# Optimization experiments

Measured on AMD Instinct MI355X. Metric: run time of the kernel, lower is better.

The kernel has to match this reference:

```python
import jax, jax.numpy as jnp
import numpy as np

# dims: F=N_fault, V=N_train (noise samples), E=batch, M=n_in+2, N=n_out
F, V, E, N_IN, N_OUT = 2, 4, 2048, 512, 512
M = N_IN + 2
GMIN, GMAX, EPS_TRAIN, PGMIN = 0.01, 10.0, 0.1, 1e-4
ETA2_ACT1 = 0.20  # ACT1.eta_fault[0,2], used in theta init
# pTanh activation params per ACT: a = e0 + e1*tanh((z-e2)*e3)
ETAS = np.array([[0.05, 0.90, 0.20, 8.0],
                 [0.10, 0.80, 0.30, 5.0],
                 [0.00, 1.00, 0.25, 10.0],
                 [0.15, 0.70, 0.15, 6.0]], dtype=np.float32)


def setup_inputs() -> dict:
    key = jax.random.key(0)
    k1, k2, k3, k4, k5 = jax.random.split(key, 5)
    a_previous = jax.random.uniform(k1, (F, V, E, N_IN), jnp.float32)
    # theta init per __init__: rand/100 + gmin; last row += gmax; row -2 from eta_2 formula
    theta = jax.random.uniform(k2, (M, N_OUT), jnp.float32) / 100.0 + GMIN
    theta = theta.at[-1, :].add(GMAX)
    theta = theta.at[-2, :].set(ETA2_ACT1 / (1.0 - ETA2_ACT1) * (jnp.sum(theta[:-2, :], 0) + theta[-1, :]))
    cofficients_act = jax.random.uniform(k3, (4, N_OUT), jnp.float32)
    noise_u = jax.random.uniform(k4, (F, V, M, N_OUT), jnp.float32)   # theta_noisy uniform draw
    gumbel_u = jax.random.uniform(k5, (4, N_OUT), jnp.float32)        # gumbel uniform draw
    return {"a_previous": a_previous, "theta_": theta,
            "cofficients_act": cofficients_act, "noise_u": noise_u, "gumbel_u": gumbel_u}


def _forward(a_previous, theta_, cofficients_act, noise_u, gumbel_u):
    sg = jax.lax.stop_gradient
    # --- theta property: clamp to [-gmax,gmax], zero |.|<gmin, straight-through ---
    th_c = jnp.clip(theta_, -GMAX, GMAX)
    th_t = jnp.where(jnp.abs(th_c) < GMIN, 0.0, th_c)
    theta = sg(th_t) + theta_ - sg(theta_)
    # --- theta_noisy: multiplicative uniform noise in [1-eps, 1+eps]; FaultMask == 1 ---
    theta_noisy = theta[None, None] * ((noise_u * 2.0 - 1.0) * EPS_TRAIN + 1.0)  # [F,V,M,N]
    absn = jnp.abs(theta_noisy)
    W = absn / (jnp.sum(absn, axis=2, keepdims=True) + 1e-10)
    pos = (theta_noisy >= 0).astype(theta_noisy.dtype)
    neg = 1.0 - pos
    # --- MAC: extend input with [ones, zeros], inverter path, split-sign matmul ---
    ones = jnp.ones(a_previous.shape[:3] + (1,), a_previous.dtype)
    zeros = jnp.zeros_like(ones)
    x_ext = jnp.concatenate([a_previous, ones, zeros], axis=3)  # [F,V,E,M]
    x_neg = (-x_ext).at[..., -1].set(0.0)                       # ideal INV(a) = -a, last col zeroed
    z = (jnp.einsum('fvem,fvmn->fven', x_ext, W * pos)
         + jnp.einsum('fvem,fvmn->fven', x_neg, W * neg))       # [F,V,E,N]
    # --- MAC_power: vectorized form of the quad loop ---
    # Power = sum_{f,v,m,n} g[m,n] * sum_e (x_ext*pos + x_neg*neg - y)^2 / (E*V*F)
    # pos*neg = 0, pos^2 = pos  =>  expand the square into einsum reductions.
    g_init = jnp.abs(th_c)
    g_tilde = g_init * (PGMIN / jnp.min(g_init, axis=0, keepdims=True))
    pos_d, neg_d = sg(pos), sg(neg)  # detached in torch source
    sx2 = jnp.einsum('fvem,fvem->fvm', x_ext, x_ext)
    sn2 = jnp.einsum('fvem,fvem->fvm', x_neg, x_neg)
    sy2 = jnp.einsum('fven,fven->fvn', z, z)
    C = jnp.einsum('fvem,fven->fvmn', x_ext, z)
    D = jnp.einsum('fvem,fven->fvmn', x_neg, z)
    p1 = (jnp.einsum('fvm,fvmn,mn->', sx2, pos_d, g_tilde)
          + jnp.einsum('fvm,fvmn,mn->', sn2, neg_d, g_tilde))
    p2 = -2.0 * (jnp.einsum('fvmn,fvmn,mn->', C, pos_d, g_tilde)
                 + jnp.einsum('fvmn,fvmn,mn->', D, neg_d, g_tilde))
    p3 = jnp.einsum('fvn,n->', sy2, jnp.sum(g_tilde, axis=0))
    mac_power = (p1 + p2 + p3) / (E * V * F)
    # --- CoFF_ACT: clamped logits + gumbel, softmax, hard argmax straight-through ---
    c = cofficients_act + sg(jnp.clip(cofficients_act, -1.0, 1.0) - cofficients_act)
    gn = -jnp.log(-jnp.log(gumbel_u + 1e-20) + 1e-20)
    alpha = jax.nn.softmax((c + gn) / 1.0, axis=0)              # temperature = 1.0
    hard = jax.nn.one_hot(jnp.argmax(alpha, axis=0), 4, axis=0, dtype=alpha.dtype)
    alpha_st = sg(hard) + alpha - sg(alpha)                      # [4, N]
    # --- mix the four pTanh activations ---
    a_new = jnp.zeros_like(z)
    for i in range(4):
        e0, e1, e2, e3 = ETAS[i]
        a_new = a_new + alpha_st[i] * (e0 + e1 * jnp.tanh((z - e2) * e3))
    return a_new, mac_power


def reference(a_previous, theta_, cofficients_act, noise_u, gumbel_u):
    return _forward(a_previous, theta_, cofficients_act, noise_u, gumbel_u)
```

## Files before the change

kernel.cpp:

```cpp
#include <hip/hip_runtime.h>

typedef unsigned short u16;
typedef __attribute__((ext_vector_type(8))) short short8;
typedef __attribute__((ext_vector_type(4))) float f32x4;

#define NF 2
#define NV 4
#define FV 8
#define NE 2048
#define NIN 512
#define NOUT 512
#define NM 514

#define WS_P1      0u
#define WS_P2      2048u
#define WS_P3      3072u
#define WS_SCALE   4096u
#define WS_G       6144u
#define WS_GN      8320u
#define WS_ETA     10368u
#define WS_DENOM   18560u
#define WS_BIASZ   34944u
#define WS_BIAST   51328u
#define WS_PMIN    67712u
#define WS_PSUM    198784u
#define WS_ABF     329856u
#define WS_BZT     17107072u
#define WS_BTT     21301376u

__constant__ float c_etas[4][4] = {
    {0.05f, 0.90f, 0.20f, 8.0f},
    {0.10f, 0.80f, 0.30f, 5.0f},
    {0.00f, 1.00f, 0.25f, 10.0f},
    {0.15f, 0.70f, 0.15f, 6.0f}};

__device__ __forceinline__ u16 f2bf(float x) {
    unsigned u = __float_as_uint(x);
    unsigned r = (u + 0x7fffu + ((u >> 16) & 1u)) >> 16;
    return (u16)r;
}

__device__ __forceinline__ void gll16(const void* g, void* l) {
    __builtin_amdgcn_global_load_lds((__attribute__((address_space(1))) void*)g,
                                     (__attribute__((address_space(3))) void*)l,
                                     16, 0, 0);
}

__global__ void kA_part(const float* __restrict__ theta_, float* __restrict__ pmin,
                        float* __restrict__ psum) {
    int t = threadIdx.x;
    int n2 = t * 2;
    int r0 = blockIdx.x * 9;
    float mn0 = 3.4e38f, mn1 = 3.4e38f, s0 = 0.f, s1 = 0.f;
    int rend = r0 + 9;
    if (rend > NM) rend = NM;
    for (int r = r0; r < rend; r++) {
        float2 v = *(const float2*)(theta_ + r * NOUT + n2);
        float a0 = fabsf(fminf(fmaxf(v.x, -10.f), 10.f));
        float a1 = fabsf(fminf(fmaxf(v.y, -10.f), 10.f));
        mn0 = fminf(mn0, a0); mn1 = fminf(mn1, a1);
        s0 += a0; s1 += a1;
    }
    *(float2*)(pmin + blockIdx.x * NOUT + n2) = make_float2(mn0, mn1);
    *(float2*)(psum + blockIdx.x * NOUT + n2) = make_float2(s0, s1);
}

__global__ void kB_fold(const float* __restrict__ pmin, const float* __restrict__ psum,
                        float* __restrict__ scale, float* __restrict__ Gn) {
    int n = threadIdx.x;
    float mn = 3.4e38f, s = 0.f;
    for (int i = 0; i < 64; i++) {
        mn = fminf(mn, pmin[i * NOUT + n]);
        s += psum[i * NOUT + n];
    }
    float sc = 1e-4f / mn;
    scale[n] = sc;
    Gn[n] = sc * s;
}

__global__ void kC_grow(const float* __restrict__ theta_, const float* __restrict__ scale,
                        float* __restrict__ G) {
    int m = blockIdx.x;
    int t = threadIdx.x;
    const float4* rowp = (const float4*)(theta_ + m * NOUT);
    const float4* scp = (const float4*)scale;
    float acc = 0.f;
#pragma unroll
    for (int i = 0; i < 2; i++) {
        float4 v = rowp[t * 2 + i];
        float4 s = scp[t * 2 + i];
        acc += fabsf(fminf(fmaxf(v.x, -10.f), 10.f)) * s.x
             + fabsf(fminf(fmaxf(v.y, -10.f), 10.f)) * s.y
             + fabsf(fminf(fmaxf(v.z, -10.f), 10.f)) * s.z
             + fabsf(fminf(fmaxf(v.w, -10.f), 10.f)) * s.w;
    }
    for (int off = 32; off > 0; off >>= 1) acc += __shfl_down(acc, off);
    if (t == 0) G[m] = acc;
}

__global__ void k_etasel(const float* __restrict__ coeff, const float* __restrict__ gumb,
                         float4* __restrict__ eta4) {
    int n = blockIdx.x * 256 + threadIdx.x;
    if (n >= NOUT) return;
    float best = -1e30f;
    int bi = 0;
    for (int i = 0; i < 4; i++) {
        float c = fminf(fmaxf(coeff[i * NOUT + n], -1.f), 1.f);
        float u = gumb[i * NOUT + n];
        float g = -logf(-logf(u + 1e-20f) + 1e-20f);
        float v = c + g;
        if (v > best) { best = v; bi = i; }
    }
    eta4[n] = make_float4(c_etas[bi][0], c_etas[bi][1], c_etas[bi][2], c_etas[bi][3]);
}

__global__ void k_denom(const float* __restrict__ theta_, const float* __restrict__ noise,
                        float* __restrict__ denom) {
    int fv = blockIdx.z, mc = blockIdx.y, nc = blockIdx.x;
    int t = threadIdx.x;
    int nl = t & 63, mg = t >> 6;
    int n = nc * 64 + nl;
    int mbase = mc * 128 + mg * 32;
    float acc = 0.f;
    for (int i = 0; i < 32; i++) {
        int m = mbase + i;
        if (m < NM) {
            float fac = noise[(fv * NM + m) * NOUT + n] * 0.2f + 0.9f;
            float thc = fminf(fmaxf(theta_[m * NOUT + n], -10.f), 10.f);
            float tht = (fabsf(thc) < 0.01f) ? 0.f : thc;
            acc += fabsf(tht * fac);
        }
    }
    __shared__ float red[256];
    red[t] = acc;
    __syncthreads();
    if (t < 64)
        atomicAdd(&denom[fv * NOUT + n], red[t] + red[t + 64] + red[t + 128] + red[t + 192]);
}

__global__ void k_wmat(const float* __restrict__ theta_, const float* __restrict__ scale,
                       const float* __restrict__ noise, const float* __restrict__ denom,
                       u16* __restrict__ BzT, u16* __restrict__ BtT,
                       float* __restrict__ bias_z, float* __restrict__ bias_t) {
    int fv = blockIdx.z, mt = blockIdx.y, nt = blockIdx.x;
    int t = threadIdx.x;
    int nl = t & 63, rg = t >> 6;
    __shared__ u16 Wl[64][68];
    __shared__ u16 Sl[64][68];
    int n = nt * 64 + nl;
    float rdv = 1.f / (denom[fv * NOUT + n] + 1e-10f);
    float sc = scale[n];
    for (int r = 0; r < 16; r++) {
        int ml = rg * 16 + r;
        int m = mt * 64 + ml;
        if (m < 513) {
            float fac = noise[(fv * NM + m) * NOUT + n] * 0.2f + 0.9f;
            float thc = fminf(fmaxf(theta_[m * NOUT + n], -10.f), 10.f);
            float gi = fabsf(thc);
            float tht = (gi < 0.01f) ? 0.f : thc;
            float th = tht * fac;
            float sg = (th >= 0.f) ? 1.f : -1.f;
            float gt = gi * sc;
            if (m == 512) {
                bias_z[fv * NOUT + n] = th * rdv;
                bias_t[fv * NOUT + n] = sg * gt;
            } else {
                Wl[ml][nl] = f2bf(th * rdv);
                Sl[ml][nl] = f2bf(sg * gt);
            }
        }
    }
    __syncthreads();
    if (mt < 8) {
        for (int r = 0; r < 16; r++) {
            int nl2 = rg * 16 + r;
            int ml2 = t & 63;
            int gidx = (fv * NOUT + nt * 64 + nl2) * NIN + mt * 64 + ml2;
            BzT[gidx] = Wl[ml2][nl2];
            BtT[gidx] = Sl[ml2][nl2];
        }
    }
}

__global__ void k_prepA(const float* __restrict__ a_prev, const float* __restrict__ G,
                        u16* __restrict__ Abf, float* __restrict__ p1slot) {
    int t = threadIdx.x;
    float acc = 0.f;
#pragma unroll
    for (int i = 0; i < 4; i++) {
        int idx = (i * 2048 + blockIdx.x) * 256 + t;
        float4 v = ((const float4*)a_prev)[idx];
        int k = (idx & 127) << 2;
        float4 g4 = *((const float4*)(G + k));
        acc += v.x * v.x * g4.x + v.y * v.y * g4.y + v.z * v.z * g4.z + v.w * v.w * g4.w;
        ushort4 o;
        o.x = f2bf(v.x); o.y = f2bf(v.y); o.z = f2bf(v.z); o.w = f2bf(v.w);
        ((ushort4*)Abf)[idx] = o;
    }
    for (int off = 32; off > 0; off >>= 1) acc += __shfl_down(acc, off);
    __shared__ float red[4];
    int lane = t & 63, wv = t >> 6;
    if (lane == 0) red[wv] = acc;
    __syncthreads();
    if (t == 0)
        atomicAdd(&p1slot[(blockIdx.x & 63) * 8], red[0] + red[1] + red[2] + red[3]);
}

__global__ __launch_bounds__(256, 2) void k_gemm(
    const u16* __restrict__ Abf, const u16* __restrict__ BzT, const u16* __restrict__ BtT,
    const float* __restrict__ bias_z, const float* __restrict__ bias_t,
    const float* __restrict__ Gn, const float4* __restrict__ eta4,
    float* __restrict__ out, float* __restrict__ p2slot, float* __restrict__ p3slot) {
    __shared__ alignas(16) u16 As[128 * 32];
    __shared__ alignas(16) u16 Bzs[128 * 32];
    __shared__ alignas(16) u16 Bts[128 * 32];
    const int tid = threadIdx.x;
    const int lane = tid & 63;
    const int wv = tid >> 6;
    const int wr = wv >> 1, wc = wv & 1;
    const int fv = blockIdx.z;
    const int e0 = blockIdx.y * 128;
    const int n0 = blockIdx.x * 128;

    const u16* Ag = Abf + (fv * NE + e0) * NIN;
    const u16* Bzg = BzT + (fv * NOUT + n0) * NIN;
    const u16* Btg = BtT + (fv * NOUT + n0) * NIN;

    f32x4 accz[4][4], acct[4][4];
#pragma unroll
    for (int i = 0; i < 4; i++)
#pragma unroll
        for (int j = 0; j < 4; j++) {
            f32x4 zz = {0.f, 0.f, 0.f, 0.f};
            accz[i][j] = zz;
            acct[i][j] = zz;
        }

    const int r0 = tid >> 2;
    const int c0 = (tid & 3) * 8;

    for (int k0 = 0; k0 < 512; k0 += 32) {
        gll16(Ag + r0 * 512 + k0 + c0, (u16*)As + tid * 8);
        gll16(Ag + (r0 + 64) * 512 + k0 + c0, (u16*)As + tid * 8 + 2048);
        gll16(Bzg + r0 * 512 + k0 + c0, (u16*)Bzs + tid * 8);
        gll16(Bzg + (r0 + 64) * 512 + k0 + c0, (u16*)Bzs + tid * 8 + 2048);
        gll16(Btg + r0 * 512 + k0 + c0, (u16*)Bts + tid * 8);
        gll16(Btg + (r0 + 64) * 512 + k0 + c0, (u16*)Bts + tid * 8 + 2048);
        __builtin_amdgcn_s_waitcnt(0);
        __syncthreads();
        const int kof = (lane >> 4) * 8;
        const int rA = wr * 64 + (lane & 15);
        const int rB = wc * 64 + (lane & 15);
        short8 af[4], bzf[4], btf[4];
#pragma unroll
        for (int i = 0; i < 4; i++) af[i] = *(const short8*)(As + (rA + i * 16) * 32 + kof);
#pragma unroll
        for (int j = 0; j < 4; j++) {
            bzf[j] = *(const short8*)(Bzs + (rB + j * 16) * 32 + kof);
            btf[j] = *(const short8*)(Bts + (rB + j * 16) * 32 + kof);
        }
#pragma unroll
        for (int i = 0; i < 4; i++)
#pragma unroll
            for (int j = 0; j < 4; j++) {
                accz[i][j] = __builtin_amdgcn_mfma_f32_16x16x32_bf16(af[i], bzf[j], accz[i][j], 0, 0, 0);
                acct[i][j] = __builtin_amdgcn_mfma_f32_16x16x32_bf16(af[i], btf[j], acct[i][j], 0, 0, 0);
            }
        __syncthreads();
    }

    float p2 = 0.f, p3 = 0.f;
    const int col = lane & 15;
    const int rowq = (lane >> 4) * 4;
#pragma unroll
    for (int j = 0; j < 4; j++) {
        int n = n0 + wc * 64 + j * 16 + col;
        float bz = bias_z[fv * NOUT + n];
        float bt = bias_t[fv * NOUT + n];
        float gnv = Gn[n];
        float4 e4 = eta4[n];
#pragma unroll
        for (int i = 0; i < 4; i++) {
            int ebase = e0 + wr * 64 + i * 16 + rowq;
#pragma unroll
            for (int r = 0; r < 4; r++) {
                float z = accz[i][j][r] + bz;
                float t = acct[i][j][r] + bt;
                p2 += z * t;
                p3 += z * z * gnv;
                float x = (z - e4.z) * e4.w;
                float ex = __expf(2.f * x);
                float th = 1.f - 2.f / (ex + 1.f);
                out[(fv * NE + ebase + r) * NOUT + n] = e4.x + e4.y * th;
            }
        }
    }
    for (int off = 32; off > 0; off >>= 1) {
        p2 += __shfl_down(p2, off);
        p3 += __shfl_down(p3, off);
    }
    __shared__ float r2[4], r3[4];
    if (lane == 0) { r2[wv] = p2; r3[wv] = p3; }
    __syncthreads();
    if (tid == 0) {
        int slot = ((blockIdx.x + blockIdx.y * 4 + blockIdx.z * 64) & 31) * 8;
        atomicAdd(&p2slot[slot], r2[0] + r2[1] + r2[2] + r2[3]);
        atomicAdd(&p3slot[slot], r3[0] + r3[1] + r3[2] + r3[3]);
    }
}

__global__ void k_final(const float* __restrict__ p1s, const float* __restrict__ p2s,
                        const float* __restrict__ p3s, const float* __restrict__ G,
                        float* __restrict__ out) {
    int t = threadIdx.x;
    float s1 = p1s[t * 8];
    float s2 = (t < 32) ? p2s[t * 8] : 0.f;
    float s3 = (t < 32) ? p3s[t * 8] : 0.f;
    for (int off = 32; off > 0; off >>= 1) {
        s1 += __shfl_down(s1, off);
        s2 += __shfl_down(s2, off);
        s3 += __shfl_down(s3, off);
    }
    if (t == 0) {
        float mp = (s1 + 16384.f * G[512] - 2.f * s2 + s3) * (1.f / 16384.f);
        out[8388608] = mp;
    }
}

extern "C" void kernel_launch(void* const* d_in, const int* in_sizes, int n_in,
                              void* d_out, int out_size, void* d_ws, size_t ws_size,
                              hipStream_t stream) {
    const float* a_prev = (const float*)d_in[0];
    const float* theta_ = (const float*)d_in[1];
    const float* coeff = (const float*)d_in[2];
    const float* noise = (const float*)d_in[3];
    const float* gumb = (const float*)d_in[4];
    float* out = (float*)d_out;
    char* w = (char*)d_ws;
    float* p1s = (float*)(w + WS_P1);
    float* p2s = (float*)(w + WS_P2);
    float* p3s = (float*)(w + WS_P3);
    float* scale = (float*)(w + WS_SCALE);
    float* G = (float*)(w + WS_G);
    float* Gn = (float*)(w + WS_GN);
    float4* eta4 = (float4*)(w + WS_ETA);
    float* denom = (float*)(w + WS_DENOM);
    float* bias_z = (float*)(w + WS_BIASZ);
    float* bias_t = (float*)(w + WS_BIAST);
    float* pmin = (float*)(w + WS_PMIN);
    float* psum = (float*)(w + WS_PSUM);
    u16* Abf = (u16*)(w + WS_ABF);
    u16* BzT = (u16*)(w + WS_BZT);
    u16* BtT = (u16*)(w + WS_BTT);

    hipMemsetAsync(w + WS_P1, 0, 4096, stream);
    hipMemsetAsync(w + WS_DENOM, 0, 16384, stream);

    kA_part<<<64, 256, 0, stream>>>(theta_, pmin, psum);
    kB_fold<<<1, 512, 0, stream>>>(pmin, psum, scale, Gn);
    kC_grow<<<514, 64, 0, stream>>>(theta_, scale, G);
    k_etasel<<<2, 256, 0, stream>>>(coeff, gumb, eta4);
    k_denom<<<dim3(8, 5, FV), 256, 0, stream>>>(theta_, noise, denom);
    k_wmat<<<dim3(8, 9, FV), 256, 0, stream>>>(theta_, scale, noise, denom,
                                               BzT, BtT, bias_z, bias_t);
    k_prepA<<<2048, 256, 0, stream>>>(a_prev, G, Abf, p1s);
    k_gemm<<<dim3(4, 16, FV), 256, 0, stream>>>(Abf, BzT, BtT, bias_z, bias_t, Gn, eta4,
                                                out, p2s, p3s);
    k_final<<<1, 64, 0, stream>>>(p1s, p2s, p3s, G, out);
}
```

Measured before the change: 165.1 us.

## Fuse denominator and weight-matrix kernels, merge eta selection, raise GEMM occupancy

```diff
diff --git a/kernel.cpp b/kernel.cpp
--- a/kernel.cpp
+++ b/kernel.cpp
@@ -19,9 +19,8 @@
 #define WS_G       6144u
 #define WS_GN      8320u
 #define WS_ETA     10368u
-#define WS_DENOM   18560u
-#define WS_BIASZ   34944u
-#define WS_BIAST   51328u
+#define WS_BIASZ   18560u
+#define WS_BIAST   34944u
 #define WS_PMIN    67712u
 #define WS_PSUM    198784u
 #define WS_ABF     329856u
@@ -66,7 +65,9 @@
 }
 
 __global__ void kB_fold(const float* __restrict__ pmin, const float* __restrict__ psum,
-                        float* __restrict__ scale, float* __restrict__ Gn) {
+                        const float* __restrict__ coeff, const float* __restrict__ gumb,
+                        float* __restrict__ scale, float* __restrict__ Gn,
+                        float4* __restrict__ eta4) {
     int n = threadIdx.x;
     float mn = 3.4e38f, s = 0.f;
     for (int i = 0; i < 64; i++) {
@@ -76,32 +77,6 @@
     float sc = 1e-4f / mn;
     scale[n] = sc;
     Gn[n] = sc * s;
-}
-
-__global__ void kC_grow(const float* __restrict__ theta_, const float* __restrict__ scale,
-                        float* __restrict__ G) {
-    int m = blockIdx.x;
-    int t = threadIdx.x;
-    const float4* rowp = (const float4*)(theta_ + m * NOUT);
-    const float4* scp = (const float4*)scale;
-    float acc = 0.f;
-#pragma unroll
-    for (int i = 0; i < 2; i++) {
-        float4 v = rowp[t * 2 + i];
-        float4 s = scp[t * 2 + i];
-        acc += fabsf(fminf(fmaxf(v.x, -10.f), 10.f)) * s.x
-             + fabsf(fminf(fmaxf(v.y, -10.f), 10.f)) * s.y
-             + fabsf(fminf(fmaxf(v.z, -10.f), 10.f)) * s.z
-             + fabsf(fminf(fmaxf(v.w, -10.f), 10.f)) * s.w;
-    }
-    for (int off = 32; off > 0; off >>= 1) acc += __shfl_down(acc, off);
-    if (t == 0) G[m] = acc;
-}
-
-__global__ void k_etasel(const float* __restrict__ coeff, const float* __restrict__ gumb,
-                         float4* __restrict__ eta4) {
-    int n = blockIdx.x * 256 + threadIdx.x;
-    if (n >= NOUT) return;
     float best = -1e30f;
     int bi = 0;
     for (int i = 0; i < 4; i++) {
@@ -114,64 +89,69 @@
     eta4[n] = make_float4(c_etas[bi][0], c_etas[bi][1], c_etas[bi][2], c_etas[bi][3]);
 }
 
-__global__ void k_denom(const float* __restrict__ theta_, const float* __restrict__ noise,
-                        float* __restrict__ denom) {
-    int fv = blockIdx.z, mc = blockIdx.y, nc = blockIdx.x;
+__global__ void kC_grow(const float* __restrict__ theta_, const float* __restrict__ scale,
+                        float* __restrict__ G) {
+    int m = blockIdx.x;
     int t = threadIdx.x;
-    int nl = t & 63, mg = t >> 6;
-    int n = nc * 64 + nl;
-    int mbase = mc * 128 + mg * 32;
+    const float4* rowp = (const float4*)(theta_ + m * NOUT);
+    const float4* scp = (const float4*)scale;
     float acc = 0.f;
-    for (int i = 0; i < 32; i++) {
-        int m = mbase + i;
-        if (m < NM) {
-            float fac = noise[(fv * NM + m) * NOUT + n] * 0.2f + 0.9f;
-            float thc = fminf(fmaxf(theta_[m * NOUT + n], -10.f), 10.f);
-            float tht = (fabsf(thc) < 0.01f) ? 0.f : thc;
-            acc += fabsf(tht * fac);
-        }
-    }
-    __shared__ float red[256];
-    red[t] = acc;
+#pragma unroll
+    for (int i = 0; i < 2; i++) {
+        float4 v = rowp[t * 2 + i];
+        float4 s = scp[t * 2 + i];
+        acc += fabsf(fminf(fmaxf(v.x, -10.f), 10.f)) * s.x
+             + fabsf(fminf(fmaxf(v.y, -10.f), 10.f)) * s.y
+             + fabsf(fminf(fmaxf(v.z, -10.f), 10.f)) * s.z
+             + fabsf(fminf(fmaxf(v.w, -10.f), 10.f)) * s.w;
+    }
+    for (int off = 32; off > 0; off >>= 1) acc += __shfl_down(acc, off);
+    if (t == 0) G[m] = acc;
+}
+
+__global__ void k_wmat2(const float* __restrict__ theta_, const float* __restrict__ scale,
+                        const float* __restrict__ noise,
+                        u16* __restrict__ BzT, u16* __restrict__ BtT,
+                        float* __restrict__ bias_z, float* __restrict__ bias_t) {
+    const int nt = blockIdx.x, fv = blockIdx.y;
+    const int t = threadIdx.x;
+    const int nl = t & 63, mg = t >> 6;
+    const int n = nt * 64 + nl;
+    float acc = 0.f;
+    for (int m = mg; m < NM; m += 4) {
+        float fac = noise[(fv * NM + m) * NOUT + n] * 0.2f + 0.9f;
+        float thc = fminf(fmaxf(theta_[m * NOUT + n], -10.f), 10.f);
+        float tht = (fabsf(thc) < 0.01f) ? 0.f : thc;
+        acc += fabsf(tht * fac);
+    }
+    __shared__ float red[4][64];
+    __shared__ float rdvl[64];
+    red[mg][nl] = acc;
     __syncthreads();
-    if (t < 64)
-        atomicAdd(&denom[fv * NOUT + n], red[t] + red[t + 64] + red[t + 128] + red[t + 192]);
-}
-
-__global__ void k_wmat(const float* __restrict__ theta_, const float* __restrict__ scale,
-                       const float* __restrict__ noise, const float* __restrict__ denom,
-                       u16* __restrict__ BzT, u16* __restrict__ BtT,
-                       float* __restrict__ bias_z, float* __restrict__ bias_t) {
-    int fv = blockIdx.z, mt = blockIdx.y, nt = blockIdx.x;
-    int t = threadIdx.x;
-    int nl = t & 63, rg = t >> 6;
-    __shared__ u16 Wl[64][68];
-    __shared__ u16 Sl[64][68];
-    int n = nt * 64 + nl;
-    float rdv = 1.f / (denom[fv * NOUT + n] + 1e-10f);
-    float sc = scale[n];
-    for (int r = 0; r < 16; r++) {
-        int ml = rg * 16 + r;
-        int m = mt * 64 + ml;
-        if (m < 513) {
+    if (mg == 0)
+        rdvl[nl] = 1.f / (red[0][nl] + red[1][nl] + red[2][nl] + red[3][nl] + 1e-10f);
+    __syncthreads();
+    const float rdv = rdvl[nl];
+    const float sc = scale[n];
+    __shared__ u16 Wl[64][66];
+    __shared__ u16 Sl[64][66];
+    const int rg = mg;
+    for (int mt = 0; mt < 8; mt++) {
+#pragma unroll
+        for (int r = 0; r < 16; r++) {
+            int ml = rg * 16 + r;
+            int m = mt * 64 + ml;
             float fac = noise[(fv * NM + m) * NOUT + n] * 0.2f + 0.9f;
             float thc = fminf(fmaxf(theta_[m * NOUT + n], -10.f), 10.f);
             float gi = fabsf(thc);
             float tht = (gi < 0.01f) ? 0.f : thc;
             float th = tht * fac;
             float sg = (th >= 0.f) ? 1.f : -1.f;
-            float gt = gi * sc;
-            if (m == 512) {
-                bias_z[fv * NOUT + n] = th * rdv;
-                bias_t[fv * NOUT + n] = sg * gt;
-            } else {
-                Wl[ml][nl] = f2bf(th * rdv);
-                Sl[ml][nl] = f2bf(sg * gt);
-            }
-        }
-    }
-    __syncthreads();
-    if (mt < 8) {
+            Wl[ml][nl] = f2bf(th * rdv);
+            Sl[ml][nl] = f2bf(sg * gi * sc);
+        }
+        __syncthreads();
+#pragma unroll
         for (int r = 0; r < 16; r++) {
             int nl2 = rg * 16 + r;
             int ml2 = t & 63;
@@ -179,6 +159,17 @@
             BzT[gidx] = Wl[ml2][nl2];
             BtT[gidx] = Sl[ml2][nl2];
         }
+        __syncthreads();
+    }
+    if (t < 64) {
+        int nn = nt * 64 + t;
+        float fac = noise[(fv * NM + 512) * NOUT + nn] * 0.2f + 0.9f;
+        float thc = fminf(fmaxf(theta_[512 * NOUT + nn], -10.f), 10.f);
+        float gi = fabsf(thc);
+        float tht = (gi < 0.01f) ? 0.f : thc;
+        float th = tht * fac;
+        bias_z[fv * NOUT + nn] = th * rdvl[t];
+        bias_t[fv * NOUT + nn] = ((th >= 0.f) ? 1.f : -1.f) * gi * scale[nn];
     }
 }
 
@@ -206,7 +197,7 @@
         atomicAdd(&p1slot[(blockIdx.x & 63) * 8], red[0] + red[1] + red[2] + red[3]);
 }
 
-__global__ __launch_bounds__(256, 2) void k_gemm(
+__global__ __launch_bounds__(256, 3) void k_gemm(
     const u16* __restrict__ Abf, const u16* __restrict__ BzT, const u16* __restrict__ BtT,
     const float* __restrict__ bias_z, const float* __restrict__ bias_t,
     const float* __restrict__ Gn, const float4* __restrict__ eta4,
@@ -251,21 +242,19 @@
         const int kof = (lane >> 4) * 8;
         const int rA = wr * 64 + (lane & 15);
         const int rB = wc * 64 + (lane & 15);
-        short8 af[4], bzf[4], btf[4];
+        short8 af[4];
 #pragma unroll
         for (int i = 0; i < 4; i++) af[i] = *(const short8*)(As + (rA + i * 16) * 32 + kof);
 #pragma unroll
         for (int j = 0; j < 4; j++) {
-            bzf[j] = *(const short8*)(Bzs + (rB + j * 16) * 32 + kof);
-            btf[j] = *(const short8*)(Bts + (rB + j * 16) * 32 + kof);
-        }
-#pragma unroll
-        for (int i = 0; i < 4; i++)
-#pragma unroll
-            for (int j = 0; j < 4; j++) {
-                accz[i][j] = __builtin_amdgcn_mfma_f32_16x16x32_bf16(af[i], bzf[j], accz[i][j], 0, 0, 0);
-                acct[i][j] = __builtin_amdgcn_mfma_f32_16x16x32_bf16(af[i], btf[j], acct[i][j], 0, 0, 0);
+            short8 bz = *(const short8*)(Bzs + (rB + j * 16) * 32 + kof);
+            short8 bt = *(const short8*)(Bts + (rB + j * 16) * 32 + kof);
+#pragma unroll
+            for (int i = 0; i < 4; i++) {
+                accz[i][j] = __builtin_amdgcn_mfma_f32_16x16x32_bf16(af[i], bz, accz[i][j], 0, 0, 0);
+                acct[i][j] = __builtin_amdgcn_mfma_f32_16x16x32_bf16(af[i], bt, acct[i][j], 0, 0, 0);
             }
+        }
         __syncthreads();
     }
 
@@ -344,7 +333,6 @@
     float* G = (float*)(w + WS_G);
     float* Gn = (float*)(w + WS_GN);
     float4* eta4 = (float4*)(w + WS_ETA);
-    float* denom = (float*)(w + WS_DENOM);
     float* bias_z = (float*)(w + WS_BIASZ);
     float* bias_t = (float*)(w + WS_BIAST);
     float* pmin = (float*)(w + WS_PMIN);
@@ -354,15 +342,11 @@
     u16* BtT = (u16*)(w + WS_BTT);
 
     hipMemsetAsync(w + WS_P1, 0, 4096, stream);
-    hipMemsetAsync(w + WS_DENOM, 0, 16384, stream);
 
     kA_part<<<64, 256, 0, stream>>>(theta_, pmin, psum);
-    kB_fold<<<1, 512, 0, stream>>>(pmin, psum, scale, Gn);
+    kB_fold<<<1, 512, 0, stream>>>(pmin, psum, coeff, gumb, scale, Gn, eta4);
     kC_grow<<<514, 64, 0, stream>>>(theta_, scale, G);
-    k_etasel<<<2, 256, 0, stream>>>(coeff, gumb, eta4);
-    k_denom<<<dim3(8, 5, FV), 256, 0, stream>>>(theta_, noise, denom);
-    k_wmat<<<dim3(8, 9, FV), 256, 0, stream>>>(theta_, scale, noise, denom,
-                                               BzT, BtT, bias_z, bias_t);
+    k_wmat2<<<dim3(8, 8), 256, 0, stream>>>(theta_, scale, noise, BzT, BtT, bias_z, bias_t);
     k_prepA<<<2048, 256, 0, stream>>>(a_prev, G, Abf, p1s);
     k_gemm<<<dim3(4, 16, FV), 256, 0, stream>>>(Abf, BzT, BtT, bias_z, bias_t, Gn, eta4,
                                                 out, p2s, p3s);
```

Result: slower. 225.8 us (+36.8%).
